# Kernel optimization log

Hardware: AMD Instinct MI355X
Metric: run time of the kernel (lower is better)

Reference implementation:

```python
import jax, jax.numpy as jnp
import numpy as np

N_NODES = 100000
N_EDGES = 1600000
IN_FEATS = 256
OUT_FEATS = 128


def setup_inputs() -> dict:
    key = jax.random.key(0)
    k1, k2, k3, k4, k5 = jax.random.split(key, 5)
    inputs = jax.random.normal(k1, (N_NODES, IN_FEATS), dtype=jnp.float32)
    # kaiming_uniform-like init for W
    bound = np.sqrt(6.0 / IN_FEATS)
    W = jax.random.uniform(k2, (IN_FEATS, OUT_FEATS), dtype=jnp.float32, minval=-bound, maxval=bound)
    B = jnp.zeros((OUT_FEATS,), dtype=jnp.float32)
    edge_src = jax.random.randint(k3, (N_EDGES,), 0, N_NODES, dtype=jnp.int32)
    edge_dst = jax.random.randint(k4, (N_EDGES,), 0, N_NODES, dtype=jnp.int32)
    # normalized-adjacency-style positive edge weights
    edge_weight = jax.random.uniform(k5, (N_EDGES,), dtype=jnp.float32)
    return {"inputs": inputs, "W": W, "B": B,
            "edge_src": edge_src, "edge_dst": edge_dst, "edge_weight": edge_weight}


def reference(inputs, W, B, edge_src, edge_dst, edge_weight):
    # support = inputs @ W  (dense GEMM)  [N, out_feats]
    support = inputs @ W
    # output = spmm(adj, support): out[dst] += w_e * support[src]
    gathered = support[edge_src] * edge_weight[:, None]        # [E, out_feats]
    output = jax.ops.segment_sum(gathered, edge_dst, num_segments=inputs.shape[0])
    return output + B
```

## Files before the change

kernel.cpp:

```cpp
#include <hip/hip_runtime.h>
#include <cstddef>

#define IN_F 256
#define OUT_F 128
#define SCAN_CHUNK 1024

__global__ __launch_bounds__(256) void gemm_kernel(const float* __restrict__ X,
                                                   const float* __restrict__ W,
                                                   float* __restrict__ S,
                                                   int nrows) {
    __shared__ float Xs[64][36];
    __shared__ float Ws[64][128];
    const int t = threadIdx.x;
    const int bm = blockIdx.x * 32;
    const int c4 = (t & 31) * 4;
    const int r4 = (t >> 5) * 4;
    float acc[4][4] = {{0.f, 0.f, 0.f, 0.f}};

    for (int kt = 0; kt < IN_F; kt += 64) {
#pragma unroll
        for (int l = 0; l < 2; ++l) {
            const int r = t & 31;
            const int km = (t >> 5) + l * 8;
            int rr = bm + r; if (rr >= nrows) rr = nrows - 1;
            const float4 v = *reinterpret_cast<const float4*>(
                &X[(size_t)rr * IN_F + kt + km * 4]);
            Xs[km * 4 + 0][r] = v.x;
            Xs[km * 4 + 1][r] = v.y;
            Xs[km * 4 + 2][r] = v.z;
            Xs[km * 4 + 3][r] = v.w;
        }
#pragma unroll
        for (int l = 0; l < 8; ++l) {
            const int q = t + l * 256;
            const int k = q >> 5;
            const int c = (q & 31) * 4;
            *reinterpret_cast<float4*>(&Ws[k][c]) =
                *reinterpret_cast<const float4*>(&W[(size_t)(kt + k) * OUT_F + c]);
        }
        __syncthreads();
#pragma unroll 8
        for (int kk = 0; kk < 64; ++kk) {
            const float4 wv = *reinterpret_cast<const float4*>(&Ws[kk][c4]);
            const float4 xv = *reinterpret_cast<const float4*>(&Xs[kk][r4]);
            acc[0][0] += xv.x * wv.x; acc[0][1] += xv.x * wv.y;
            acc[0][2] += xv.x * wv.z; acc[0][3] += xv.x * wv.w;
            acc[1][0] += xv.y * wv.x; acc[1][1] += xv.y * wv.y;
            acc[1][2] += xv.y * wv.z; acc[1][3] += xv.y * wv.w;
            acc[2][0] += xv.z * wv.x; acc[2][1] += xv.z * wv.y;
            acc[2][2] += xv.z * wv.z; acc[2][3] += xv.z * wv.w;
            acc[3][0] += xv.w * wv.x; acc[3][1] += xv.w * wv.y;
            acc[3][2] += xv.w * wv.z; acc[3][3] += xv.w * wv.w;
        }
        __syncthreads();
    }
#pragma unroll
    for (int j = 0; j < 4; ++j) {
        const int row = bm + r4 + j;
        if (row < nrows) {
            const float4 o = make_float4(acc[j][0], acc[j][1], acc[j][2], acc[j][3]);
            *reinterpret_cast<float4*>(&S[(size_t)row * OUT_F + c4]) = o;
        }
    }
}

__global__ void hist_kernel(const int* __restrict__ dst, int* __restrict__ counts, int E) {
    int i = blockIdx.x * blockDim.x + threadIdx.x;
    const int stride = gridDim.x * blockDim.x;
    for (; i < E; i += stride) atomicAdd(&counts[dst[i]], 1);
}

__global__ __launch_bounds__(256) void scan1_kernel(const int* __restrict__ counts,
                                                    int* __restrict__ off,
                                                    int* __restrict__ bsums, int n) {
    __shared__ int sd[256];
    const int t = threadIdx.x;
    const int base = blockIdx.x * SCAN_CHUNK + t * 4;
    int c[4]; int s = 0;
#pragma unroll
    for (int j = 0; j < 4; ++j) {
        c[j] = (base + j < n) ? counts[base + j] : 0;
        s += c[j];
    }
    sd[t] = s;
    __syncthreads();
    for (int d = 1; d < 256; d <<= 1) {
        int v = (t >= d) ? sd[t - d] : 0;
        __syncthreads();
        sd[t] += v;
        __syncthreads();
    }
    int run = sd[t] - s;
#pragma unroll
    for (int j = 0; j < 4; ++j) {
        if (base + j < n) off[base + j] = run;
        run += c[j];
    }
    if (t == 255) bsums[blockIdx.x] = sd[255];
}

__global__ __launch_bounds__(256) void scan2_kernel(int* __restrict__ bsums, int nb) {
    __shared__ int sd[256];
    const int t = threadIdx.x;
    const int v = (t < nb) ? bsums[t] : 0;
    sd[t] = v;
    __syncthreads();
    for (int d = 1; d < 256; d <<= 1) {
        int u = (t >= d) ? sd[t - d] : 0;
        __syncthreads();
        sd[t] += u;
        __syncthreads();
    }
    if (t < nb) bsums[t] = sd[t] - v;
}

__global__ __launch_bounds__(256) void scan3_kernel(int* __restrict__ off,
                                                    int* __restrict__ cursor,
                                                    const int* __restrict__ bsums,
                                                    int n, int total) {
    const int t = threadIdx.x;
    const int base = blockIdx.x * SCAN_CHUNK + t * 4;
    const int add = bsums[blockIdx.x];
#pragma unroll
    for (int j = 0; j < 4; ++j) {
        const int idx = base + j;
        if (idx < n) {
            const int v = off[idx] + add;
            off[idx] = v;
            cursor[idx] = v;
        }
    }
    if (blockIdx.x == 0 && t == 0) off[n] = total;
}

__global__ void scatter_kernel(const int* __restrict__ src, const int* __restrict__ dst,
                               const float* __restrict__ w, int* __restrict__ cursor,
                               int2* __restrict__ pairs, int E) {
    int i = blockIdx.x * blockDim.x + threadIdx.x;
    const int stride = gridDim.x * blockDim.x;
    for (; i < E; i += stride) {
        const int d = dst[i];
        const int pos = atomicAdd(&cursor[d], 1);
        int2 p;
        p.x = src[i];
        p.y = __float_as_int(w[i]);
        pairs[pos] = p;
    }
}

__global__ __launch_bounds__(256) void gather_kernel(const float* __restrict__ S,
                                                     const int* __restrict__ off,
                                                     const int2* __restrict__ pairs,
                                                     const float* __restrict__ B,
                                                     float* __restrict__ out, int n) {
    const int node = blockIdx.x * 2 + (threadIdx.x >> 7);
    const int f = threadIdx.x & 127;
    if (node >= n) return;
    const int s = off[node];
    const int e = off[node + 1];
    float acc0 = 0.f, acc1 = 0.f;
    int i = s;
    for (; i + 1 < e; i += 2) {
        const int2 p0 = pairs[i];
        const int2 p1 = pairs[i + 1];
        acc0 += __int_as_float(p0.y) * S[(size_t)p0.x * OUT_F + f];
        acc1 += __int_as_float(p1.y) * S[(size_t)p1.x * OUT_F + f];
    }
    if (i < e) {
        const int2 p = pairs[i];
        acc0 += __int_as_float(p.y) * S[(size_t)p.x * OUT_F + f];
    }
    out[(size_t)node * OUT_F + f] = acc0 + acc1 + B[f];
}

__global__ void init_out_kernel(float* __restrict__ out, const float* __restrict__ B, size_t n) {
    size_t i = (size_t)blockIdx.x * blockDim.x + threadIdx.x;
    const size_t stride = (size_t)gridDim.x * blockDim.x;
    for (; i < n; i += stride) out[i] = B[i & (OUT_F - 1)];
}

__global__ void atomic_scatter_kernel(const float* __restrict__ S, const int* __restrict__ src,
                                      const int* __restrict__ dst, const float* __restrict__ w,
                                      float* __restrict__ out, int E) {
    size_t i = (size_t)blockIdx.x * blockDim.x + threadIdx.x;
    const size_t stride = (size_t)gridDim.x * blockDim.x;
    const size_t total = (size_t)E * OUT_F;
    for (; i < total; i += stride) {
        const int e = (int)(i >> 7);
        const int f = (int)(i & 127);
        atomicAdd(&out[(size_t)dst[e] * OUT_F + f], w[e] * S[(size_t)src[e] * OUT_F + f]);
    }
}

extern "C" void kernel_launch(void* const* d_in, const int* in_sizes, int n_in,
                              void* d_out, int out_size, void* d_ws, size_t ws_size,
                              hipStream_t stream) {
    const float* X    = (const float*)d_in[0];
    const float* W    = (const float*)d_in[1];
    const float* B    = (const float*)d_in[2];
    const int*   esrc = (const int*)d_in[3];
    const int*   edst = (const int*)d_in[4];
    const float* ew   = (const float*)d_in[5];
    float* out = (float*)d_out;

    const int N = in_sizes[0] / IN_F;
    const int E = in_sizes[3];

    char* ws = (char*)d_ws;
    size_t cur = 0;
    auto carve = [&](size_t bytes) -> void* {
        void* p = ws + cur;
        cur = (cur + bytes + 255) & ~(size_t)255;
        return p;
    };
    float* support = (float*)carve((size_t)N * OUT_F * sizeof(float));
    int*   counts  = (int*)carve((size_t)N * sizeof(int));
    int*   offs    = (int*)carve((size_t)(N + 1) * sizeof(int));
    int*   cursor  = (int*)carve((size_t)N * sizeof(int));
    int*   bsums   = (int*)carve(1024 * sizeof(int));
    int2*  pairs   = (int2*)carve((size_t)E * sizeof(int2));
    const bool csr_ok = (cur <= ws_size);

    const int gemm_grid = (N + 31) / 32;
    gemm_kernel<<<gemm_grid, 256, 0, stream>>>(X, W, support, N);

    if (csr_ok) {
        hipMemsetAsync(counts, 0, (size_t)N * sizeof(int), stream);
        hist_kernel<<<1024, 256, 0, stream>>>(edst, counts, E);
        const int nb = (N + SCAN_CHUNK - 1) / SCAN_CHUNK;
        scan1_kernel<<<nb, 256, 0, stream>>>(counts, offs, bsums, N);
        scan2_kernel<<<1, 256, 0, stream>>>(bsums, nb);
        scan3_kernel<<<nb, 256, 0, stream>>>(offs, cursor, bsums, N, E);
        scatter_kernel<<<1024, 256, 0, stream>>>(esrc, edst, ew, cursor, pairs, E);
        gather_kernel<<<(N + 1) / 2, 256, 0, stream>>>(support, offs, pairs, B, out, N);
    } else {
        init_out_kernel<<<2048, 256, 0, stream>>>(out, B, (size_t)N * OUT_F);
        atomic_scatter_kernel<<<4096, 256, 0, stream>>>(support, esrc, edst, ew, out, E);
    }
}
```

Baseline: 621.8 us.

## Enlarge GEMM register tile and vectorize CSR gather with float2 per lane

The GEMM now computes a 64-row tile with each thread holding an 8x4 accumulator block and a K-step of 32, raising arithmetic per shared-memory load. The gather kernel now assigns 64 lanes per node, each handling two features via float2 loads, and unrolls four edges per iteration to expose more memory-level parallelism. The histogram and scatter grids are doubled. The larger register tile raises register pressure and the 64-row tiles halve the GEMM grid, which may reduce occupancy.

```diff
diff --git a/kernel.cpp b/kernel.cpp
--- a/kernel.cpp
+++ b/kernel.cpp
@@ -9,29 +9,30 @@
                                                    const float* __restrict__ W,
                                                    float* __restrict__ S,
                                                    int nrows) {
-    __shared__ float Xs[64][36];
-    __shared__ float Ws[64][128];
-    const int t = threadIdx.x;
-    const int bm = blockIdx.x * 32;
-    const int c4 = (t & 31) * 4;
-    const int r4 = (t >> 5) * 4;
-    float acc[4][4] = {{0.f, 0.f, 0.f, 0.f}};
-
-    for (int kt = 0; kt < IN_F; kt += 64) {
+    __shared__ float Xs[32][68];
+    __shared__ float Ws[32][128];
+    const int t = threadIdx.x;
+    const int bm = blockIdx.x * 64;
+    const int tr = (t >> 5) * 8;
+    const int tc = (t & 31) * 4;
+    float acc[8][4] = {};
+
+    for (int kt = 0; kt < IN_F; kt += 32) {
 #pragma unroll
         for (int l = 0; l < 2; ++l) {
-            const int r = t & 31;
-            const int km = (t >> 5) + l * 8;
+            const int idx = t + l * 256;
+            const int r = idx >> 3;
+            const int k4 = idx & 7;
             int rr = bm + r; if (rr >= nrows) rr = nrows - 1;
             const float4 v = *reinterpret_cast<const float4*>(
-                &X[(size_t)rr * IN_F + kt + km * 4]);
-            Xs[km * 4 + 0][r] = v.x;
-            Xs[km * 4 + 1][r] = v.y;
-            Xs[km * 4 + 2][r] = v.z;
-            Xs[km * 4 + 3][r] = v.w;
-        }
-#pragma unroll
-        for (int l = 0; l < 8; ++l) {
+                &X[(size_t)rr * IN_F + kt + k4 * 4]);
+            Xs[k4 * 4 + 0][r] = v.x;
+            Xs[k4 * 4 + 1][r] = v.y;
+            Xs[k4 * 4 + 2][r] = v.z;
+            Xs[k4 * 4 + 3][r] = v.w;
+        }
+#pragma unroll
+        for (int l = 0; l < 4; ++l) {
             const int q = t + l * 256;
             const int k = q >> 5;
             const int c = (q & 31) * 4;
@@ -39,27 +40,28 @@
                 *reinterpret_cast<const float4*>(&W[(size_t)(kt + k) * OUT_F + c]);
         }
         __syncthreads();
-#pragma unroll 8
-        for (int kk = 0; kk < 64; ++kk) {
-            const float4 wv = *reinterpret_cast<const float4*>(&Ws[kk][c4]);
-            const float4 xv = *reinterpret_cast<const float4*>(&Xs[kk][r4]);
-            acc[0][0] += xv.x * wv.x; acc[0][1] += xv.x * wv.y;
-            acc[0][2] += xv.x * wv.z; acc[0][3] += xv.x * wv.w;
-            acc[1][0] += xv.y * wv.x; acc[1][1] += xv.y * wv.y;
-            acc[1][2] += xv.y * wv.z; acc[1][3] += xv.y * wv.w;
-            acc[2][0] += xv.z * wv.x; acc[2][1] += xv.z * wv.y;
-            acc[2][2] += xv.z * wv.z; acc[2][3] += xv.z * wv.w;
-            acc[3][0] += xv.w * wv.x; acc[3][1] += xv.w * wv.y;
-            acc[3][2] += xv.w * wv.z; acc[3][3] += xv.w * wv.w;
-        }
-        __syncthreads();
-    }
-#pragma unroll
-    for (int j = 0; j < 4; ++j) {
-        const int row = bm + r4 + j;
+#pragma unroll 4
+        for (int kk = 0; kk < 32; ++kk) {
+            const float4 x0 = *reinterpret_cast<const float4*>(&Xs[kk][tr]);
+            const float4 x1 = *reinterpret_cast<const float4*>(&Xs[kk][tr + 4]);
+            const float4 wv = *reinterpret_cast<const float4*>(&Ws[kk][tc]);
+            const float xr[8] = {x0.x, x0.y, x0.z, x0.w, x1.x, x1.y, x1.z, x1.w};
+#pragma unroll
+            for (int j = 0; j < 8; ++j) {
+                acc[j][0] += xr[j] * wv.x;
+                acc[j][1] += xr[j] * wv.y;
+                acc[j][2] += xr[j] * wv.z;
+                acc[j][3] += xr[j] * wv.w;
+            }
+        }
+        __syncthreads();
+    }
+#pragma unroll
+    for (int j = 0; j < 8; ++j) {
+        const int row = bm + tr + j;
         if (row < nrows) {
-            const float4 o = make_float4(acc[j][0], acc[j][1], acc[j][2], acc[j][3]);
-            *reinterpret_cast<float4*>(&S[(size_t)row * OUT_F + c4]) = o;
+            *reinterpret_cast<float4*>(&S[(size_t)row * OUT_F + tc]) =
+                make_float4(acc[j][0], acc[j][1], acc[j][2], acc[j][3]);
         }
     }
 }
@@ -153,24 +155,42 @@
                                                      const int2* __restrict__ pairs,
                                                      const float* __restrict__ B,
                                                      float* __restrict__ out, int n) {
-    const int node = blockIdx.x * 2 + (threadIdx.x >> 7);
-    const int f = threadIdx.x & 127;
+    const int node = blockIdx.x * 4 + (threadIdx.x >> 6);
+    const int lane = threadIdx.x & 63;
     if (node >= n) return;
-    const int s = off[node];
+    int i = off[node];
     const int e = off[node + 1];
-    float acc0 = 0.f, acc1 = 0.f;
-    int i = s;
-    for (; i + 1 < e; i += 2) {
+    const size_t fo = (size_t)lane * 2;
+    float ax = 0.f, ay = 0.f, bx = 0.f, by = 0.f;
+    for (; i + 4 <= e; i += 4) {
         const int2 p0 = pairs[i];
         const int2 p1 = pairs[i + 1];
-        acc0 += __int_as_float(p0.y) * S[(size_t)p0.x * OUT_F + f];
-        acc1 += __int_as_float(p1.y) * S[(size_t)p1.x * OUT_F + f];
-    }
-    if (i < e) {
+        const int2 p2 = pairs[i + 2];
+        const int2 p3 = pairs[i + 3];
+        const float2 v0 = *reinterpret_cast<const float2*>(&S[(size_t)p0.x * OUT_F + fo]);
+        const float2 v1 = *reinterpret_cast<const float2*>(&S[(size_t)p1.x * OUT_F + fo]);
+        const float2 v2 = *reinterpret_cast<const float2*>(&S[(size_t)p2.x * OUT_F + fo]);
+        const float2 v3 = *reinterpret_cast<const float2*>(&S[(size_t)p3.x * OUT_F + fo]);
+        const float w0 = __int_as_float(p0.y);
+        const float w1 = __int_as_float(p1.y);
+        const float w2 = __int_as_float(p2.y);
+        const float w3 = __int_as_float(p3.y);
+        ax += w0 * v0.x; ay += w0 * v0.y;
+        bx += w1 * v1.x; by += w1 * v1.y;
+        ax += w2 * v2.x; ay += w2 * v2.y;
+        bx += w3 * v3.x; by += w3 * v3.y;
+    }
+    for (; i < e; ++i) {
         const int2 p = pairs[i];
-        acc0 += __int_as_float(p.y) * S[(size_t)p.x * OUT_F + f];
-    }
-    out[(size_t)node * OUT_F + f] = acc0 + acc1 + B[f];
+        const float2 v = *reinterpret_cast<const float2*>(&S[(size_t)p.x * OUT_F + fo]);
+        const float w = __int_as_float(p.y);
+        ax += w * v.x; ay += w * v.y;
+    }
+    const float2 b2 = *reinterpret_cast<const float2*>(&B[fo]);
+    float2 o;
+    o.x = ax + bx + b2.x;
+    o.y = ay + by + b2.y;
+    *reinterpret_cast<float2*>(&out[(size_t)node * OUT_F + fo]) = o;
 }
 
 __global__ void init_out_kernel(float* __restrict__ out, const float* __restrict__ B, size_t n) {
@@ -221,18 +241,18 @@
     int2*  pairs   = (int2*)carve((size_t)E * sizeof(int2));
     const bool csr_ok = (cur <= ws_size);
 
-    const int gemm_grid = (N + 31) / 32;
+    const int gemm_grid = (N + 63) / 64;
     gemm_kernel<<<gemm_grid, 256, 0, stream>>>(X, W, support, N);
 
     if (csr_ok) {
         hipMemsetAsync(counts, 0, (size_t)N * sizeof(int), stream);
-        hist_kernel<<<1024, 256, 0, stream>>>(edst, counts, E);
+        hist_kernel<<<2048, 256, 0, stream>>>(edst, counts, E);
         const int nb = (N + SCAN_CHUNK - 1) / SCAN_CHUNK;
         scan1_kernel<<<nb, 256, 0, stream>>>(counts, offs, bsums, N);
         scan2_kernel<<<1, 256, 0, stream>>>(bsums, nb);
         scan3_kernel<<<nb, 256, 0, stream>>>(offs, cursor, bsums, N, E);
-        scatter_kernel<<<1024, 256, 0, stream>>>(esrc, edst, ew, cursor, pairs, E);
-        gather_kernel<<<(N + 1) / 2, 256, 0, stream>>>(support, offs, pairs, B, out, N);
+        scatter_kernel<<<2048, 256, 0, stream>>>(esrc, edst, ew, cursor, pairs, E);
+        gather_kernel<<<(N + 3) / 4, 256, 0, stream>>>(support, offs, pairs, B, out, N);
     } else {
         init_out_kernel<<<2048, 256, 0, stream>>>(out, B, (size_t)N * OUT_F);
         atomic_scatter_kernel<<<4096, 256, 0, stream>>>(support, esrc, edst, ew, out, E);
```

Measured after the change: 547.0 us. -12.0%, faster.
